# Kernel optimization log

Hardware: AMD Instinct MI355X
Metric: run time of the kernel (lower is better)

The kernel has to match this reference:

```python
import jax, jax.numpy as jnp
import numpy as np

N_PAIRS = 500000
L = 4          # l_max + 1
S = 4          # number of species
N_MAX = 16     # n_max per l (uniform)
HID = 32       # MLP hidden width


def setup_inputs() -> dict:
    key = jax.random.key(0)
    ks = jax.random.split(key, 6)
    radial_functions = jax.random.normal(ks[0], (N_PAIRS, L * N_MAX), dtype=jnp.float32)
    species = jax.random.randint(ks[1], (N_PAIRS,), 0, S, dtype=jnp.int64)
    # per-(l, species) MLP weights, stored as [L, S, in, out]; 0.3 scale keeps SiLU well-behaved
    W1 = jax.random.normal(ks[2], (L, S, N_MAX, HID), dtype=jnp.float32) * 0.3
    W2 = jax.random.normal(ks[3], (L, S, HID, HID), dtype=jnp.float32) * 0.3
    W3 = jax.random.normal(ks[4], (L, S, HID, HID), dtype=jnp.float32) * 0.3
    W4 = jax.random.normal(ks[5], (L, S, HID, N_MAX), dtype=jnp.float32) * 0.3
    return {"radial_functions": radial_functions, "species": species,
            "W1": W1, "W2": W2, "W3": W3, "W4": W4}


def reference(radial_functions, species, W1, W2, W3, W4):
    # torch.split(radial_functions, n_max_l, dim=1) with uniform n_max_l == reshape
    n = radial_functions.shape[0]
    x = radial_functions.reshape(n, L, N_MAX)              # [N, L, n_max]
    onehot = jax.nn.one_hot(species, S, dtype=x.dtype)      # [N, S]
    out = jnp.zeros_like(x)
    # per-species MLP applied to the rows of that species (gather-MLP-scatter),
    # expressed as dense compute + one-hot masking (S is tiny, MLPs are tiny)
    for s in range(S):
        h = jax.nn.silu(jnp.einsum('nli,lio->nlo', x, W1[:, s]))   # [N, L, 32]
        h = jax.nn.silu(jnp.einsum('nli,lio->nlo', h, W2[:, s]))
        h = jax.nn.silu(jnp.einsum('nli,lio->nlo', h, W3[:, s]))
        y = jnp.einsum('nli,lio->nlo', h, W4[:, s])                # [N, L, n_max]
        out = out + onehot[:, s][:, None, None] * y
    return out  # equivalent to the list of per-l tensors, stacked along axis 1
```

## Files before the change

kernel.cpp:

```cpp
#include <hip/hip_runtime.h>
#include <stdint.h>

typedef unsigned int u32;
typedef unsigned long long u64;

constexpr int L   = 4;
constexpr int S   = 4;
constexpr int NM  = 16;
constexpr int HID = 32;
constexpr int BLK = 256;
constexpr int NFRAG = 7;
constexpr int WF_ENTRIES = L * S * NFRAG * 64;
constexpr int WS_PERM_INT = (256 + WF_ENTRIES * 16) / 4;

typedef short  s16x8  __attribute__((ext_vector_type(8)));
typedef float  f32x16 __attribute__((ext_vector_type(16)));
typedef float  f32x4  __attribute__((ext_vector_type(4)));
typedef unsigned int u32x2 __attribute__((ext_vector_type(2)));


__device__ __forceinline__ int load_species(const int* sp, int i64, int n) {
    return i64 ? sp[2 * n] : sp[n];
}

__global__ void k_wprep(const void* __restrict__ W1, const void* __restrict__ W2,
                        const void* __restrict__ W3, const void* __restrict__ W4,
                        const u32* __restrict__ rfw, int* __restrict__ hdr,
                        uint4* __restrict__ wf) {
    __shared__ int sf32;
    int tid = threadIdx.x;
    if (tid < 64) {
        u32 w  = rfw[tid];
        u32 lo = w & 0xffffu;
        u32 ex = (lo >> 7) & 0xffu;
        int plausible = (lo == 0u || (ex >= 90u && ex <= 141u)) ? 1 : 0;
        u64 pm = __ballot(plausible);
        if (tid == 0) sf32 = (__popcll(pm) < 48) ? 1 : 0;
    }
    if (blockIdx.x == 0 && tid < 9) hdr[tid] = 0;
    __syncthreads();
    int isf32 = sf32;

    int e = blockIdx.x * BLK + tid;
    if (e >= WF_ENTRIES) return;
    int lam = e & 63;
    int f   = (e >> 6) % NFRAG;
    int ls  = e / (64 * NFRAG);
    int m = lam & 31, h = lam >> 5;
    unsigned short vals[8];
#pragma unroll
    for (int j = 0; j < 8; j++) {
        int k = 8 * h + j;
        const void* base; size_t off; bool zero = false;
        if (f == 0)      { base = W1; off = (size_t)ls * 512  + (size_t)k * 32 + m; }
        else if (f <= 2) { base = W2; off = (size_t)ls * 1024 + (size_t)(k + 16 * (f - 1)) * 32 + m; }
        else if (f <= 4) { base = W3; off = (size_t)ls * 1024 + (size_t)(k + 16 * (f - 3)) * 32 + m; }
        else             { zero = (m >= NM); base = W4;
                           off = (size_t)ls * 512 + (size_t)(k + 16 * (f - 5)) * NM + (m & 15); }
        unsigned short v;
        if (zero) v = 0;
        else if (isf32) {
            u32 u = __float_as_uint(((const float*)base)[off]);
            u32 r = ((u >> 16) & 1u) + 0x7fffu;
            v = (unsigned short)((u + r) >> 16);
        } else v = ((const unsigned short*)base)[off];
        vals[j] = v;
    }
    uint4 q;
    q.x = vals[0] | ((u32)vals[1] << 16);
    q.y = vals[2] | ((u32)vals[3] << 16);
    q.z = vals[4] | ((u32)vals[5] << 16);
    q.w = vals[6] | ((u32)vals[7] << 16);
    wf[e] = q;
}

__global__ void k1_hist(const int* __restrict__ sp, int* __restrict__ hdr, int N) {
    __shared__ int cnt[S];
    __shared__ int si64;
    int t = threadIdx.x;
    if (t < 64) {
        u64 om = __ballot(((const u32*)sp)[2 * t + 1] != 0u);
        if (t == 0) si64 = (om == 0ull) ? 1 : 0;
    }
    if (t < S) cnt[t] = 0;
    __syncthreads();
    int i64 = si64;
    int base = blockIdx.x * (BLK * 4) + t * 4;
    if (base + 3 < N) {
        int s0, s1, s2, s3;
        if (i64) {
            int4 a = ((const int4*)sp)[base / 2];
            int4 b = ((const int4*)sp)[base / 2 + 1];
            s0 = a.x; s1 = a.z; s2 = b.x; s3 = b.z;
        } else {
            int4 a = ((const int4*)sp)[base / 4];
            s0 = a.x; s1 = a.y; s2 = a.z; s3 = a.w;
        }
        atomicAdd(&cnt[s0], 1); atomicAdd(&cnt[s1], 1);
        atomicAdd(&cnt[s2], 1); atomicAdd(&cnt[s3], 1);
    } else {
        for (int k = 0; k < 4; k++) {
            int n = base + k;
            if (n < N) atomicAdd(&cnt[load_species(sp, i64, n)], 1);
        }
    }
    __syncthreads();
    if (t < S) atomicAdd(&hdr[t], cnt[t]);
}

__global__ void k3_scatter(const int* __restrict__ sp, int* __restrict__ hdr,
                           int* __restrict__ perm, int N) {
    __shared__ int cnt[S];
    __shared__ int base[S];
    __shared__ int bp[S + 1];
    __shared__ int cs[S];
    __shared__ int si64;
    int t = threadIdx.x;
    if (t < 64) {
        u64 om = __ballot(((const u32*)sp)[2 * t + 1] != 0u);
        if (t == 0) si64 = (om == 0ull) ? 1 : 0;
    }
    if (t == 0) {
        int acc = 0;
        for (int q = 0; q < S; q++) {
            cs[q] = hdr[q];
            bp[q] = acc;
            acc += (cs[q] + BLK - 1) & ~(BLK - 1);
        }
        bp[S] = acc;
    }
    if (t < S) cnt[t] = 0;
    __syncthreads();
    int i64 = si64;
    int nb0 = blockIdx.x * (BLK * 4) + t * 4;
    int s_[4], r_[4];
    bool v_[4];
    if (nb0 + 3 < N) {
        if (i64) {
            int4 a = ((const int4*)sp)[nb0 / 2];
            int4 b = ((const int4*)sp)[nb0 / 2 + 1];
            s_[0] = a.x; s_[1] = a.z; s_[2] = b.x; s_[3] = b.z;
        } else {
            int4 a = ((const int4*)sp)[nb0 / 4];
            s_[0] = a.x; s_[1] = a.y; s_[2] = a.z; s_[3] = a.w;
        }
        v_[0] = v_[1] = v_[2] = v_[3] = true;
    } else {
        for (int k = 0; k < 4; k++) {
            int n = nb0 + k;
            v_[k] = (n < N);
            s_[k] = v_[k] ? load_species(sp, i64, n) : 0;
        }
    }
#pragma unroll
    for (int k = 0; k < 4; k++)
        if (v_[k]) r_[k] = atomicAdd(&cnt[s_[k]], 1);
    __syncthreads();
    if (t < S) base[t] = bp[t] + atomicAdd(&hdr[4 + t], cnt[t]);
    __syncthreads();
#pragma unroll
    for (int k = 0; k < 4; k++)
        if (v_[k]) perm[base[s_[k]] + r_[k]] = nb0 + k;
    if (blockIdx.x == 0) {
        for (int q = 0; q < S; q++)
            for (int i = bp[q] + cs[q] + t; i < bp[q + 1]; i += BLK) perm[i] = -1;
    }
}

__device__ __forceinline__ u32 cvt_pk_bf16(float a, float b) {
    u32 r;
    asm("v_cvt_pk_bf16_f32 %0, %1, %2" : "=v"(r) : "v"(a), "v"(b));
    return r;
}

__device__ __forceinline__ float silu(float v) {
    float e = __expf(-v);
    return v * __builtin_amdgcn_rcpf(1.0f + e);
}

__device__ __forceinline__ void d_to_b(const f32x16& d, s16x8& Ba, s16x8& Bb) {
    u32 P[8];
#pragma unroll
    for (int i = 0; i < 8; i++)
        P[i] = cvt_pk_bf16(silu(d[2 * i]), silu(d[2 * i + 1]));
    u32x2 r02 = __builtin_amdgcn_permlane32_swap(P[0], P[2], false, false);
    u32x2 r13 = __builtin_amdgcn_permlane32_swap(P[1], P[3], false, false);
    u32x2 r46 = __builtin_amdgcn_permlane32_swap(P[4], P[6], false, false);
    u32x2 r57 = __builtin_amdgcn_permlane32_swap(P[5], P[7], false, false);
    Ba = __builtin_bit_cast(s16x8, make_uint4(r02[0], r13[0], r02[1], r13[1]));
    Bb = __builtin_bit_cast(s16x8, make_uint4(r46[0], r57[0], r46[1], r57[1]));
}

__device__ __forceinline__ s16x8 bf16pack4(uint4 q0, uint4 q1) {
    u32 w0 = cvt_pk_bf16(__uint_as_float(q0.x), __uint_as_float(q0.y));
    u32 w1 = cvt_pk_bf16(__uint_as_float(q0.z), __uint_as_float(q0.w));
    u32 w2 = cvt_pk_bf16(__uint_as_float(q1.x), __uint_as_float(q1.y));
    u32 w3 = cvt_pk_bf16(__uint_as_float(q1.z), __uint_as_float(q1.w));
    return __builtin_bit_cast(s16x8, make_uint4(w0, w1, w2, w3));
}

constexpr int SCW = 36;

__global__ __launch_bounds__(BLK, 4) void k4_mlp(
    const void* __restrict__ rf, const int* __restrict__ hdr,
    const int* __restrict__ perm, const uint4* __restrict__ wf,
    void* __restrict__ outp)
{
    __shared__ uint4 lw[L * NFRAG * 64];
    __shared__ float sc[4][16 * SCW];
    __shared__ int   sn[4][2][32];
    __shared__ int   sf32;

    int tid = threadIdx.x;

    int c0 = hdr[0], c1 = hdr[1], c2 = hdr[2], c3 = hdr[3];
    int b1 = (c0 + BLK - 1) & ~(BLK - 1);
    int b2 = b1 + ((c1 + BLK - 1) & ~(BLK - 1));
    int b3 = b2 + ((c2 + BLK - 1) & ~(BLK - 1));
    int b4 = b3 + ((c3 + BLK - 1) & ~(BLK - 1));
    int p0 = blockIdx.x * BLK;
    if (p0 >= b4) return;
    int s = (p0 >= b3) ? 3 : ((p0 >= b2) ? 2 : ((p0 >= b1) ? 1 : 0));
    s = __builtin_amdgcn_readfirstlane(s);

    if (tid < 64) {
        u32 w  = ((const u32*)rf)[tid];
        u32 lo = w & 0xffffu;
        u32 ex = (lo >> 7) & 0xffu;
        int plausible = (lo == 0u || (ex >= 90u && ex <= 141u)) ? 1 : 0;
        u64 pm = __ballot(plausible);
        if (tid == 0) sf32 = (__popcll(pm) < 48) ? 1 : 0;
    }

#pragma unroll
    for (int c = 0; c < 7; c++) {
        int idx = tid + c * BLK;
        int l = idx / (NFRAG * 64);
        int r = idx - l * (NFRAG * 64);
        lw[idx] = wf[(size_t)((l * S + s) * NFRAG) * 64 + r];
    }

    int wv   = tid >> 6;
    int lane = tid & 63;
    int col  = lane & 31;
    int h    = lane >> 5;

    int n_t[2];
#pragma unroll
    for (int t = 0; t < 2; t++) {
        n_t[t] = perm[p0 + wv * 64 + t * 32 + col];
        sn[wv][t][col] = n_t[t];
    }
    __syncthreads();
    int isf32 = sf32;

    if (isf32) {
        const char* xb = (const char*)rf;
        int nn0 = n_t[0] < 0 ? 0 : n_t[0];
        int nn1 = n_t[1] < 0 ? 0 : n_t[1];
        const uint4* rp0 = (const uint4*)(xb + (size_t)nn0 * 256 + h * 32);
        const uint4* rp1 = (const uint4*)(xb + (size_t)nn1 * 256 + h * 32);

        int rg = lane >> 3;
        int cc = lane & 7;
        int bh = col >> 4;
        int pr = col & 15;
        float* scb = &sc[wv][0];

        uint4 rawb[2][4];
        rawb[0][0] = rp0[0]; rawb[0][1] = rp0[1];
        rawb[0][2] = rp0[4]; rawb[0][3] = rp0[5];

#pragma unroll
        for (int j = 0; j < 4; j++) {
            int lp = j >> 1, t = j & 1;
            if (j < 3) {
                int jn = j + 1;
                int lpn = jn >> 1, tn = jn & 1;
                const uint4* pl = tn ? rp1 : rp0;
                rawb[jn & 1][0] = pl[lpn * 8 + 0];
                rawb[jn & 1][1] = pl[lpn * 8 + 1];
                rawb[jn & 1][2] = pl[lpn * 8 + 4];
                rawb[jn & 1][3] = pl[lpn * 8 + 5];
            }
            int lA = 2 * lp, lB = 2 * lp + 1;
            s16x8 frA[NFRAG], frB[NFRAG];
#pragma unroll
            for (int f = 0; f < NFRAG; f++) {
                frA[f] = __builtin_bit_cast(s16x8, lw[(lA * NFRAG + f) * 64 + lane]);
                frB[f] = __builtin_bit_cast(s16x8, lw[(lB * NFRAG + f) * 64 + lane]);
            }

            s16x8 B1A = bf16pack4(rawb[j & 1][0], rawb[j & 1][1]);
            s16x8 B1B = bf16pack4(rawb[j & 1][2], rawb[j & 1][3]);

            f32x16 z = {0.0f};
            f32x16 dA = __builtin_amdgcn_mfma_f32_32x32x16_bf16(frA[0], B1A, z, 0, 0, 0);
            f32x16 dB = __builtin_amdgcn_mfma_f32_32x32x16_bf16(frB[0], B1B, z, 0, 0, 0);

            s16x8 BaA, BbA, BaB, BbB;
            d_to_b(dA, BaA, BbA);
            d_to_b(dB, BaB, BbB);
            dA = __builtin_amdgcn_mfma_f32_32x32x16_bf16(frA[1], BaA, z, 0, 0, 0);
            dB = __builtin_amdgcn_mfma_f32_32x32x16_bf16(frB[1], BaB, z, 0, 0, 0);
            dA = __builtin_amdgcn_mfma_f32_32x32x16_bf16(frA[2], BbA, dA, 0, 0, 0);
            dB = __builtin_amdgcn_mfma_f32_32x32x16_bf16(frB[2], BbB, dB, 0, 0, 0);

            d_to_b(dA, BaA, BbA);
            d_to_b(dB, BaB, BbB);
            dA = __builtin_amdgcn_mfma_f32_32x32x16_bf16(frA[3], BaA, z, 0, 0, 0);
            dB = __builtin_amdgcn_mfma_f32_32x32x16_bf16(frB[3], BaB, z, 0, 0, 0);
            dA = __builtin_amdgcn_mfma_f32_32x32x16_bf16(frA[4], BbA, dA, 0, 0, 0);
            dB = __builtin_amdgcn_mfma_f32_32x32x16_bf16(frB[4], BbB, dB, 0, 0, 0);

            d_to_b(dA, BaA, BbA);
            d_to_b(dB, BaB, BbB);
            dA = __builtin_amdgcn_mfma_f32_32x32x16_bf16(frA[5], BaA, z, 0, 0, 0);
            dB = __builtin_amdgcn_mfma_f32_32x32x16_bf16(frB[5], BaB, z, 0, 0, 0);
            dA = __builtin_amdgcn_mfma_f32_32x32x16_bf16(frA[6], BbA, dA, 0, 0, 0);
            dB = __builtin_amdgcn_mfma_f32_32x32x16_bf16(frB[6], BbB, dB, 0, 0, 0);

#pragma unroll
            for (int b = 0; b < 2; b++) {
                if (bh == b) {
                    float* swA = scb + pr * SCW + 4 * h;
                    *(f32x4*)swA        = (f32x4){dA[0], dA[1], dA[2], dA[3]};
                    *(f32x4*)(swA + 8)  = (f32x4){dA[4], dA[5], dA[6], dA[7]};
                    float* swB = swA + 16;
                    *(f32x4*)swB        = (f32x4){dB[0], dB[1], dB[2], dB[3]};
                    *(f32x4*)(swB + 8)  = (f32x4){dB[4], dB[5], dB[6], dB[7]};
                }
                asm volatile("s_waitcnt lgkmcnt(0)" ::: "memory");
                __builtin_amdgcn_sched_barrier(0);

#pragma unroll
                for (int i = 0; i < 2; i++) {
                    int lr = 8 * i + rg;
                    int r  = 16 * b + lr;
                    int n  = sn[wv][t][r];
                    const float* srd = scb + lr * SCW + 4 * cc;
                    f32x4 v = *(const f32x4*)srd;
                    if (n >= 0)
                        *(f32x4*)((char*)outp + (size_t)n * 256 + (size_t)lp * 128 + cc * 16) = v;
                }
                asm volatile("s_waitcnt lgkmcnt(0)" ::: "memory");
                __builtin_amdgcn_sched_barrier(0);
            }
        }
    } else {
#pragma unroll
        for (int l = 0; l < L; l++) {
            s16x8 fr[NFRAG];
#pragma unroll
            for (int f = 0; f < NFRAG; f++)
                fr[f] = __builtin_bit_cast(s16x8, lw[(l * NFRAG + f) * 64 + lane]);

#pragma unroll
            for (int t = 0; t < 2; t++) {
                int n = n_t[t];
                int nn = n < 0 ? 0 : n;

                const char* xb = (const char*)rf;
                s16x8 B1 = __builtin_bit_cast(s16x8,
                     *(const uint4*)(xb + (size_t)nn * 128 + l * 32 + h * 16));

                f32x16 z = {0.0f};
                f32x16 d1 = __builtin_amdgcn_mfma_f32_32x32x16_bf16(fr[0], B1, z, 0, 0, 0);

                s16x8 Ba, Bb;
                d_to_b(d1, Ba, Bb);
                f32x16 d2 = __builtin_amdgcn_mfma_f32_32x32x16_bf16(fr[1], Ba, z, 0, 0, 0);
                d2 = __builtin_amdgcn_mfma_f32_32x32x16_bf16(fr[2], Bb, d2, 0, 0, 0);

                d_to_b(d2, Ba, Bb);
                f32x16 d3 = __builtin_amdgcn_mfma_f32_32x32x16_bf16(fr[3], Ba, z, 0, 0, 0);
                d3 = __builtin_amdgcn_mfma_f32_32x32x16_bf16(fr[4], Bb, d3, 0, 0, 0);

                d_to_b(d3, Ba, Bb);
                f32x16 d4 = __builtin_amdgcn_mfma_f32_32x32x16_bf16(fr[5], Ba, z, 0, 0, 0);
                d4 = __builtin_amdgcn_mfma_f32_32x32x16_bf16(fr[6], Bb, d4, 0, 0, 0);

                u32 P[4];
#pragma unroll
                for (int i = 0; i < 4; i++) P[i] = cvt_pk_bf16(d4[2 * i], d4[2 * i + 1]);
                u32x2 r02 = __builtin_amdgcn_permlane32_swap(P[0], P[2], false, false);
                u32x2 r13 = __builtin_amdgcn_permlane32_swap(P[1], P[3], false, false);
                if (n >= 0) {
                    uint4 v = make_uint4(r02[0], r13[0], r02[1], r13[1]);
                    char* ob = (char*)outp;
                    *(uint4*)(ob + (size_t)n * 128 + l * 32 + h * 16) = v;
                }
            }
        }
    }
}

extern "C" void kernel_launch(void* const* d_in, const int* in_sizes, int n_in,
                              void* d_out, int out_size, void* d_ws, size_t ws_size,
                              hipStream_t stream) {
    const void* rf     = d_in[0];
    const int* species = (const int*)d_in[1];
    const void* W1     = d_in[2];
    const void* W2     = d_in[3];
    const void* W3     = d_in[4];
    const void* W4     = d_in[5];

    int N = in_sizes[1];
    int* hdr   = (int*)d_ws;
    uint4* wf  = (uint4*)((char*)d_ws + 256);
    int* perm  = (int*)d_ws + WS_PERM_INT;

    int nb4   = (N + BLK * 4 - 1) / (BLK * 4);
    int nwp   = (WF_ENTRIES + BLK - 1) / BLK;
    int grid4 = (N + S * (BLK - 1) + BLK - 1) / BLK;

    k_wprep   <<<dim3(nwp),  dim3(BLK), 0, stream>>>(W1, W2, W3, W4,
                                                     (const u32*)rf, hdr, wf);
    k1_hist   <<<dim3(nb4),  dim3(BLK), 0, stream>>>(species, hdr, N);
    k3_scatter<<<dim3(nb4),  dim3(BLK), 0, stream>>>(species, hdr, perm, N);
    k4_mlp    <<<dim3(grid4),dim3(BLK), 0, stream>>>(rf, hdr, perm, wf, d_out);
}
```

Measured before the change: 273.0 us.

## Split MLP blocks across l-pairs to halve LDS weights and double grid

Each MLP block now handles only one pair of l values (chosen by the low bit of blockIdx), so the grid doubles and each block stages only two l's worth of weight fragments in LDS. The launch bound rises from 4 to 6 waves per SIMD to allow more resident blocks. This aims to raise occupancy and shorten per-block serial work, at the cost of re-reading the permutation indices and species header twice and more block launch overhead.

```diff
diff --git a/kernel.cpp b/kernel.cpp
--- a/kernel.cpp
+++ b/kernel.cpp
@@ -201,24 +201,26 @@
 
 constexpr int SCW = 36;
 
-__global__ __launch_bounds__(BLK, 4) void k4_mlp(
+__global__ __launch_bounds__(BLK, 6) void k4_mlp(
     const void* __restrict__ rf, const int* __restrict__ hdr,
     const int* __restrict__ perm, const uint4* __restrict__ wf,
     void* __restrict__ outp)
 {
-    __shared__ uint4 lw[L * NFRAG * 64];
+    __shared__ uint4 lw[2 * NFRAG * 64];
     __shared__ float sc[4][16 * SCW];
     __shared__ int   sn[4][2][32];
     __shared__ int   sf32;
 
     int tid = threadIdx.x;
+    int pb  = blockIdx.x >> 1;
+    int lp  = blockIdx.x & 1;
 
     int c0 = hdr[0], c1 = hdr[1], c2 = hdr[2], c3 = hdr[3];
     int b1 = (c0 + BLK - 1) & ~(BLK - 1);
     int b2 = b1 + ((c1 + BLK - 1) & ~(BLK - 1));
     int b3 = b2 + ((c2 + BLK - 1) & ~(BLK - 1));
     int b4 = b3 + ((c3 + BLK - 1) & ~(BLK - 1));
-    int p0 = blockIdx.x * BLK;
+    int p0 = pb * BLK;
     if (p0 >= b4) return;
     int s = (p0 >= b3) ? 3 : ((p0 >= b2) ? 2 : ((p0 >= b1) ? 1 : 0));
     s = __builtin_amdgcn_readfirstlane(s);
@@ -233,11 +235,14 @@
     }
 
 #pragma unroll
-    for (int c = 0; c < 7; c++) {
+    for (int c = 0; c < 4; c++) {
         int idx = tid + c * BLK;
-        int l = idx / (NFRAG * 64);
-        int r = idx - l * (NFRAG * 64);
-        lw[idx] = wf[(size_t)((l * S + s) * NFRAG) * 64 + r];
+        if (idx < 2 * NFRAG * 64) {
+            int l2 = idx / (NFRAG * 64);
+            int r  = idx - l2 * (NFRAG * 64);
+            int l  = lp * 2 + l2;
+            lw[idx] = wf[(size_t)((l * S + s) * NFRAG) * 64 + r];
+        }
     }
 
     int wv   = tid >> 6;
@@ -258,8 +263,8 @@
         const char* xb = (const char*)rf;
         int nn0 = n_t[0] < 0 ? 0 : n_t[0];
         int nn1 = n_t[1] < 0 ? 0 : n_t[1];
-        const uint4* rp0 = (const uint4*)(xb + (size_t)nn0 * 256 + h * 32);
-        const uint4* rp1 = (const uint4*)(xb + (size_t)nn1 * 256 + h * 32);
+        const uint4* rp0 = (const uint4*)(xb + (size_t)nn0 * 256 + lp * 128 + h * 32);
+        const uint4* rp1 = (const uint4*)(xb + (size_t)nn1 * 256 + lp * 128 + h * 32);
 
         int rg = lane >> 3;
         int cc = lane & 7;
@@ -272,27 +277,20 @@
         rawb[0][2] = rp0[4]; rawb[0][3] = rp0[5];
 
 #pragma unroll
-        for (int j = 0; j < 4; j++) {
-            int lp = j >> 1, t = j & 1;
-            if (j < 3) {
-                int jn = j + 1;
-                int lpn = jn >> 1, tn = jn & 1;
-                const uint4* pl = tn ? rp1 : rp0;
-                rawb[jn & 1][0] = pl[lpn * 8 + 0];
-                rawb[jn & 1][1] = pl[lpn * 8 + 1];
-                rawb[jn & 1][2] = pl[lpn * 8 + 4];
-                rawb[jn & 1][3] = pl[lpn * 8 + 5];
+        for (int t = 0; t < 2; t++) {
+            if (t == 0) {
+                rawb[1][0] = rp1[0]; rawb[1][1] = rp1[1];
+                rawb[1][2] = rp1[4]; rawb[1][3] = rp1[5];
             }
-            int lA = 2 * lp, lB = 2 * lp + 1;
             s16x8 frA[NFRAG], frB[NFRAG];
 #pragma unroll
             for (int f = 0; f < NFRAG; f++) {
-                frA[f] = __builtin_bit_cast(s16x8, lw[(lA * NFRAG + f) * 64 + lane]);
-                frB[f] = __builtin_bit_cast(s16x8, lw[(lB * NFRAG + f) * 64 + lane]);
+                frA[f] = __builtin_bit_cast(s16x8, lw[(0 * NFRAG + f) * 64 + lane]);
+                frB[f] = __builtin_bit_cast(s16x8, lw[(1 * NFRAG + f) * 64 + lane]);
             }
 
-            s16x8 B1A = bf16pack4(rawb[j & 1][0], rawb[j & 1][1]);
-            s16x8 B1B = bf16pack4(rawb[j & 1][2], rawb[j & 1][3]);
+            s16x8 B1A = bf16pack4(rawb[t][0], rawb[t][1]);
+            s16x8 B1B = bf16pack4(rawb[t][2], rawb[t][3]);
 
             f32x16 z = {0.0f};
             f32x16 dA = __builtin_amdgcn_mfma_f32_32x32x16_bf16(frA[0], B1A, z, 0, 0, 0);
@@ -349,11 +347,12 @@
         }
     } else {
 #pragma unroll
-        for (int l = 0; l < L; l++) {
+        for (int l2 = 0; l2 < 2; l2++) {
+            int l = lp * 2 + l2;
             s16x8 fr[NFRAG];
 #pragma unroll
             for (int f = 0; f < NFRAG; f++)
-                fr[f] = __builtin_bit_cast(s16x8, lw[(l * NFRAG + f) * 64 + lane]);
+                fr[f] = __builtin_bit_cast(s16x8, lw[(l2 * NFRAG + f) * 64 + lane]);
 
 #pragma unroll
             for (int t = 0; t < 2; t++) {
@@ -412,7 +411,8 @@
 
     int nb4   = (N + BLK * 4 - 1) / (BLK * 4);
     int nwp   = (WF_ENTRIES + BLK - 1) / BLK;
-    int grid4 = (N + S * (BLK - 1) + BLK - 1) / BLK;
+    int nbp   = (N + S * (BLK - 1) + BLK - 1) / BLK;
+    int grid4 = 2 * nbp;
 
     k_wprep   <<<dim3(nwp),  dim3(BLK), 0, stream>>>(W1, W2, W3, W4,
                                                      (const u32*)rf, hdr, wf);
```

After: 277.1 us. No clear change (+1.5%).

## Replace atomic species bucketing with per-block counts, scan, and stable wave prefix

Applied to the files above, without the earlier changes.

The histogram kernel now writes per-block species counts to a table instead of atomically adding to a global header. A new single-block scan kernel turns those counts into per-block base offsets and totals. The scatter kernel computes ranks with a packed 16-bit wave shuffle prefix scan instead of LDS and global atomics, so the permutation is deterministic and ordered. This removes global atomic contention and makes each block's perm writes contiguous, at the cost of one extra kernel launch. The scratch table sits at the tail of the output buffer, which k4_mlp overwrites later.

```diff
diff --git a/kernel.cpp b/kernel.cpp
--- a/kernel.cpp
+++ b/kernel.cpp
@@ -74,7 +74,8 @@
     wf[e] = q;
 }
 
-__global__ void k1_hist(const int* __restrict__ sp, int* __restrict__ hdr, int N) {
+__global__ void k1_hist(const int* __restrict__ sp, int* __restrict__ bcnt,
+                        int N, int NB) {
     __shared__ int cnt[S];
     __shared__ int si64;
     int t = threadIdx.x;
@@ -105,17 +106,48 @@
         }
     }
     __syncthreads();
-    if (t < S) atomicAdd(&hdr[t], cnt[t]);
-}
-
-__global__ void k3_scatter(const int* __restrict__ sp, int* __restrict__ hdr,
-                           int* __restrict__ perm, int N) {
-    __shared__ int cnt[S];
-    __shared__ int base[S];
+    if (t < S) bcnt[t * NB + blockIdx.x] = cnt[t];
+}
+
+__global__ void k2_scan(int* __restrict__ hdr, int* __restrict__ bbase, int NB) {
+    int t = threadIdx.x, wv = t >> 6, lane = t & 63;
+    if (wv < S) {
+        int carry = 0;
+        for (int c0 = 0; c0 < NB; c0 += 64) {
+            int b = c0 + lane;
+            int own = (b < NB) ? bbase[wv * NB + b] : 0;
+            int x = own;
+#pragma unroll
+            for (int o = 1; o < 64; o <<= 1) {
+                int v = __shfl_up(x, o, 64);
+                if (lane >= o) x += v;
+            }
+            if (b < NB) bbase[wv * NB + b] = carry + x - own;
+            carry += __shfl(x, 63, 64);
+        }
+        if (lane == 0) hdr[wv] = carry;
+    }
+    __syncthreads();
+    int c0 = hdr[0], c1 = hdr[1], c2 = hdr[2];
+    int rb1 = (c0 + BLK - 1) & ~(BLK - 1);
+    int rb2 = rb1 + ((c1 + BLK - 1) & ~(BLK - 1));
+    int rb3 = rb2 + ((c2 + BLK - 1) & ~(BLK - 1));
+    for (int i = t; i < S * NB; i += 256) {
+        int s = i / NB;
+        int rb = (s == 0) ? 0 : ((s == 1) ? rb1 : ((s == 2) ? rb2 : rb3));
+        bbase[i] += rb;
+    }
+}
+
+__global__ void k3_scatter(const int* __restrict__ sp, const int* __restrict__ hdr,
+                           const int* __restrict__ bbase, int* __restrict__ perm,
+                           int N, int NB) {
+    __shared__ int wt01[4], wt23[4];
+    __shared__ int sbase[S];
     __shared__ int bp[S + 1];
     __shared__ int cs[S];
     __shared__ int si64;
-    int t = threadIdx.x;
+    int t = threadIdx.x, wv = t >> 6, lane = t & 63;
     if (t < 64) {
         u64 om = __ballot(((const u32*)sp)[2 * t + 1] != 0u);
         if (t == 0) si64 = (om == 0ull) ? 1 : 0;
@@ -129,11 +161,11 @@
         }
         bp[S] = acc;
     }
-    if (t < S) cnt[t] = 0;
+    if (t < S) sbase[t] = bbase[t * NB + blockIdx.x];
     __syncthreads();
     int i64 = si64;
     int nb0 = blockIdx.x * (BLK * 4) + t * 4;
-    int s_[4], r_[4];
+    int s_[4];
     bool v_[4];
     if (nb0 + 3 < N) {
         if (i64) {
@@ -152,15 +184,40 @@
             s_[k] = v_[k] ? load_species(sp, i64, n) : 0;
         }
     }
-#pragma unroll
-    for (int k = 0; k < 4; k++)
-        if (v_[k]) r_[k] = atomicAdd(&cnt[s_[k]], 1);
-    __syncthreads();
-    if (t < S) base[t] = bp[t] + atomicAdd(&hdr[4 + t], cnt[t]);
-    __syncthreads();
-#pragma unroll
-    for (int k = 0; k < 4; k++)
-        if (v_[k]) perm[base[s_[k]] + r_[k]] = nb0 + k;
+    int own01 = 0, own23 = 0;
+#pragma unroll
+    for (int k = 0; k < 4; k++) {
+        if (v_[k]) {
+            if (s_[k] < 2) own01 += 1 << (16 * s_[k]);
+            else           own23 += 1 << (16 * (s_[k] - 2));
+        }
+    }
+    int p01 = own01, p23 = own23;
+#pragma unroll
+    for (int o = 1; o < 64; o <<= 1) {
+        int v0 = __shfl_up(p01, o, 64);
+        int v1 = __shfl_up(p23, o, 64);
+        if (lane >= o) { p01 += v0; p23 += v1; }
+    }
+    if (lane == 63) { wt01[wv] = p01; wt23[wv] = p23; }
+    __syncthreads();
+    int cw01 = 0, cw23 = 0;
+    for (int w = 0; w < wv; w++) { cw01 += wt01[w]; cw23 += wt23[w]; }
+    int e01 = cw01 + p01 - own01;
+    int e23 = cw23 + p23 - own23;
+    int o0 = e01 & 0xffff, o1 = (e01 >> 16) & 0xffff;
+    int o2 = e23 & 0xffff, o3 = (e23 >> 16) & 0xffff;
+#pragma unroll
+    for (int k = 0; k < 4; k++) {
+        if (v_[k]) {
+            int s = s_[k];
+            int off = (s == 0) ? o0 : ((s == 1) ? o1 : ((s == 2) ? o2 : o3));
+            int sb  = (s == 0) ? sbase[0] : ((s == 1) ? sbase[1]
+                      : ((s == 2) ? sbase[2] : sbase[3]));
+            perm[sb + off] = nb0 + k;
+            o0 += (s == 0); o1 += (s == 1); o2 += (s == 2); o3 += (s == 3);
+        }
+    }
     if (blockIdx.x == 0) {
         for (int q = 0; q < S; q++)
             for (int i = bp[q] + cs[q] + t; i < bp[q + 1]; i += BLK) perm[i] = -1;
@@ -414,9 +471,12 @@
     int nwp   = (WF_ENTRIES + BLK - 1) / BLK;
     int grid4 = (N + S * (BLK - 1) + BLK - 1) / BLK;
 
+    int* bbase = (int*)((char*)d_out + out_size) - (size_t)S * nb4;
+
     k_wprep   <<<dim3(nwp),  dim3(BLK), 0, stream>>>(W1, W2, W3, W4,
                                                      (const u32*)rf, hdr, wf);
-    k1_hist   <<<dim3(nb4),  dim3(BLK), 0, stream>>>(species, hdr, N);
-    k3_scatter<<<dim3(nb4),  dim3(BLK), 0, stream>>>(species, hdr, perm, N);
+    k1_hist   <<<dim3(nb4),  dim3(BLK), 0, stream>>>(species, bbase, N, nb4);
+    k2_scan   <<<dim3(1),    dim3(BLK), 0, stream>>>(hdr, bbase, nb4);
+    k3_scatter<<<dim3(nb4),  dim3(BLK), 0, stream>>>(species, hdr, bbase, perm, N, nb4);
     k4_mlp    <<<dim3(grid4),dim3(BLK), 0, stream>>>(rf, hdr, perm, wf, d_out);
 }
```

New measurement: 269.7 us. About the same (-1.2%).
